# Kernel optimization log

Hardware: AMD Instinct MI355X
Metric: run time of the kernel (lower is better)

The kernel has to match this reference:

```python
import jax, jax.numpy as jnp
import numpy as np

B, N, D, H, K = 8, 128, 256, 128, 8

def setup_inputs() -> dict:
    key = jax.random.key(0)
    ks = jax.random.split(key, 6)
    E = jax.random.normal(ks[0], (B, N, D), dtype=jnp.float32)
    # kaiming_uniform-like init for linear weights
    lim1 = np.sqrt(6.0 / (2 * D))
    W1 = jax.random.uniform(ks[1], (H, 2 * D), minval=-lim1, maxval=lim1, dtype=jnp.float32)
    b1 = jnp.zeros((H,), dtype=jnp.float32)
    lim2 = np.sqrt(6.0 / H)
    W2 = jax.random.uniform(ks[2], (D, H), minval=-lim2, maxval=lim2, dtype=jnp.float32)
    b2 = jnp.zeros((D,), dtype=jnp.float32)
    q = jax.random.normal(ks[3], (K, D), dtype=jnp.float32) * (1.0 / D ** 0.5)
    return {"E": E, "W1": W1, "b1": b1, "W2": W2, "b2": b2, "q": q}

def reference(E, W1, b1, W2, b2, q):
    # phi(cat(Ei,Ej)) == relu(E_i @ W1a^T + E_j @ W1b^T + b1) @ W2^T + b2
    # Split first linear's weight to avoid materializing the [B,N,N,2D] concat.
    W1a, W1b = W1[:, :D], W1[:, D:]          # each [H, D]
    Ai = jnp.einsum('bnd,hd->bnh', E, W1a)   # [B,N,H] (row half)
    Aj = jnp.einsum('bnd,hd->bnh', E, W1b)   # [B,N,H] (col half)
    hidden = jax.nn.relu(Ai[:, :, None, :] + Aj[:, None, :, :] + b1)  # [B,N,N,H]
    # dropout is identity at inference
    # Fuse second linear with query dot: (hidden @ W2^T + b2) . q_h
    #   = hidden @ (W2^T q_h) + b2.q_h
    Wq = jnp.einsum('dh,kd->hk', W2, q)      # [H, K]
    bq = jnp.einsum('d,kd->k', b2, q)        # [K]
    logits = jnp.einsum('bijh,hk->bijh'[:0] or 'bijh,hk->bijk', hidden, Wq) + bq  # [B,N,N,K]
    M = jax.nn.sigmoid(logits).transpose(0, 3, 1, 2)  # [B,K,N,N]
    eye = jnp.eye(N, dtype=M.dtype)[None, None]
    return M * (1.0 - eye)
```

## Files before the change

kernel.cpp:

```cpp
#include <hip/hip_runtime.h>

#define PB 8
#define PN 128
#define PD 256
#define PH 128
#define PK 8
#define D2 (2*PD)

__global__ __launch_bounds__(256) void k0_prep(
        const float* __restrict__ W1, const float* __restrict__ W2,
        const float* __restrict__ b2, const float* __restrict__ q,
        float4* __restrict__ W1t4, float* __restrict__ Wq, float* __restrict__ bq)
{
    const int blk = blockIdx.x, t = threadIdx.x;
    if (blk < 64) {
        __shared__ float sm[32][33];
        const int h0 = (blk >> 4) * 32;
        const int d0 = (blk & 15) * 32;
        const int tx = t & 31, ty = t >> 5;
        #pragma unroll
        for (int r = 0; r < 4; ++r)
            sm[ty + 8 * r][tx] = W1[(h0 + ty + 8 * r) * D2 + d0 + tx];
        __syncthreads();
        const int hl = t & 31, dql = t >> 5;
        float4 w = make_float4(sm[hl][dql * 4 + 0], sm[hl][dql * 4 + 1],
                               sm[hl][dql * 4 + 2], sm[hl][dql * 4 + 3]);
        W1t4[((d0 >> 2) + dql) * PH + h0 + hl] = w;
    } else {
        __shared__ float qs[PD];
        __shared__ float red[256];
        const int k = blk - 64;
        qs[t] = q[k * PD + t];
        __syncthreads();
        if (t < PH) {
            float acc = 0.f;
            #pragma unroll 4
            for (int d = 0; d < PD; ++d)
                acc = fmaf(W2[d * PH + t], qs[d], acc);
            Wq[t * PK + k] = acc;
        }
        red[t] = b2[t] * qs[t];
        __syncthreads();
        for (int st = 128; st > 0; st >>= 1) {
            if (t < st) red[t] += red[t + st];
            __syncthreads();
        }
        if (t == 0) bq[k] = red[0];
    }
}

__global__ __launch_bounds__(256) void k1_proj(
        const float* __restrict__ E, const float* __restrict__ b1,
        const float4* __restrict__ W1t4,
        float* __restrict__ Ai, float* __restrict__ Ajt)
{
    __shared__ float es[8 * PD];
    const int blk = blockIdx.x, t = threadIdx.x;
    const int b    = blk >> 5;
    const int part = (blk >> 4) & 1;
    const int ng   = blk & 15;
    const int h    = t & (PH - 1);
    const int s    = t >> 7;

    const float* eb = E + (b * PN + ng * 8) * PD;
    #pragma unroll
    for (int r = 0; r < 8; ++r) es[r * PD + t] = eb[r * PD + t];
    __syncthreads();

    const float4* wp = W1t4 + (part * 64) * PH + h;
    const float* e0 = es + (s * 4 + 0) * PD;
    const float* e1 = e0 + PD;
    const float* e2 = e1 + PD;
    const float* e3 = e2 + PD;

    float a0 = 0.f, a1 = 0.f, a2 = 0.f, a3 = 0.f;
    #pragma unroll 4
    for (int dq = 0; dq < 64; ++dq) {
        const float4 w  = wp[dq * PH];
        const float4 p0 = *reinterpret_cast<const float4*>(e0 + dq * 4);
        const float4 p1 = *reinterpret_cast<const float4*>(e1 + dq * 4);
        const float4 p2 = *reinterpret_cast<const float4*>(e2 + dq * 4);
        const float4 p3 = *reinterpret_cast<const float4*>(e3 + dq * 4);
        a0 = fmaf(w.x, p0.x, a0); a0 = fmaf(w.y, p0.y, a0);
        a0 = fmaf(w.z, p0.z, a0); a0 = fmaf(w.w, p0.w, a0);
        a1 = fmaf(w.x, p1.x, a1); a1 = fmaf(w.y, p1.y, a1);
        a1 = fmaf(w.z, p1.z, a1); a1 = fmaf(w.w, p1.w, a1);
        a2 = fmaf(w.x, p2.x, a2); a2 = fmaf(w.y, p2.y, a2);
        a2 = fmaf(w.z, p2.z, a2); a2 = fmaf(w.w, p2.w, a2);
        a3 = fmaf(w.x, p3.x, a3); a3 = fmaf(w.y, p3.y, a3);
        a3 = fmaf(w.z, p3.z, a3); a3 = fmaf(w.w, p3.w, a3);
    }

    const int n0 = ng * 8 + s * 4;
    if (part == 0) {
        const float bb = b1[h];
        Ai[(b * PN + n0 + 0) * PH + h] = a0 + bb;
        Ai[(b * PN + n0 + 1) * PH + h] = a1 + bb;
        Ai[(b * PN + n0 + 2) * PH + h] = a2 + bb;
        Ai[(b * PN + n0 + 3) * PH + h] = a3 + bb;
    } else {
        *reinterpret_cast<float4*>(&Ajt[(b * PH + h) * PN + n0]) =
            make_float4(a0, a1, a2, a3);
    }
}

__global__ __launch_bounds__(256) void k2_score(
        const float* __restrict__ Ai, const float* __restrict__ Ajt,
        const float* __restrict__ Wq, const float* __restrict__ bq,
        float* __restrict__ out)
{
    __shared__ float  ais[4 * PH];
    __shared__ float4 wqs[2 * PH];
    __shared__ float  bqs[PK];

    const int blk = blockIdx.x, t = threadIdx.x;
    const int b  = blk >> 5;
    const int ig = blk & 31;
    const int i0 = ig * 4;
    const int il = t >> 6;
    const int jb = t & 63;

    ais[t]       = Ai[(b * PN + i0) * PH + t];
    ais[256 + t] = Ai[(b * PN + i0) * PH + 256 + t];
    wqs[t] = reinterpret_cast<const float4*>(Wq)[t];
    if (t < PK) bqs[t] = bq[t];
    __syncthreads();

    const float* ail = ais + il * PH;
    const float* ajr = Ajt + b * PH * PN + jb;

    float acc0[PK], acc1[PK];
    #pragma unroll
    for (int k = 0; k < PK; ++k) { acc0[k] = bqs[k]; acc1[k] = bqs[k]; }

    #pragma unroll 4
    for (int hh = 0; hh < PH; ++hh) {
        const float a  = ail[hh];
        const float g0 = ajr[hh * PN];
        const float g1 = ajr[hh * PN + 64];
        const float v0 = fmaxf(a + g0, 0.f);
        const float v1 = fmaxf(a + g1, 0.f);
        const float4 wA = wqs[hh * 2];
        const float4 wB = wqs[hh * 2 + 1];
        acc0[0] = fmaf(v0, wA.x, acc0[0]); acc0[1] = fmaf(v0, wA.y, acc0[1]);
        acc0[2] = fmaf(v0, wA.z, acc0[2]); acc0[3] = fmaf(v0, wA.w, acc0[3]);
        acc0[4] = fmaf(v0, wB.x, acc0[4]); acc0[5] = fmaf(v0, wB.y, acc0[5]);
        acc0[6] = fmaf(v0, wB.z, acc0[6]); acc0[7] = fmaf(v0, wB.w, acc0[7]);
        acc1[0] = fmaf(v1, wA.x, acc1[0]); acc1[1] = fmaf(v1, wA.y, acc1[1]);
        acc1[2] = fmaf(v1, wA.z, acc1[2]); acc1[3] = fmaf(v1, wA.w, acc1[3]);
        acc1[4] = fmaf(v1, wB.x, acc1[4]); acc1[5] = fmaf(v1, wB.y, acc1[5]);
        acc1[6] = fmaf(v1, wB.z, acc1[6]); acc1[7] = fmaf(v1, wB.w, acc1[7]);
    }

    const int i = i0 + il;
    #pragma unroll
    for (int k = 0; k < PK; ++k) {
        float s0 = 1.f / (1.f + __expf(-acc0[k]));
        float s1 = 1.f / (1.f + __expf(-acc1[k]));
        if (jb == i)      s0 = 0.f;
        if (jb + 64 == i) s1 = 0.f;
        float* orow = out + ((b * PK + k) * PN + i) * PN;
        orow[jb]      = s0;
        orow[jb + 64] = s1;
    }
}

extern "C" void kernel_launch(void* const* d_in, const int* in_sizes, int n_in,
                              void* d_out, int out_size, void* d_ws, size_t ws_size,
                              hipStream_t stream) {
    const float* E  = (const float*)d_in[0];
    const float* W1 = (const float*)d_in[1];
    const float* b1 = (const float*)d_in[2];
    const float* W2 = (const float*)d_in[3];
    const float* b2 = (const float*)d_in[4];
    const float* q  = (const float*)d_in[5];

    float*  Ai   = (float*)d_ws;
    float*  Ajt  = Ai + PB * PN * PH;
    float4* W1t4 = (float4*)(Ajt + PB * PH * PN);
    float*  Wq   = (float*)(W1t4 + 128 * PH);
    float*  bq   = Wq + PH * PK;

    k0_prep<<<72,  256, 0, stream>>>(W1, W2, b2, q, W1t4, Wq, bq);
    k1_proj<<<256, 256, 0, stream>>>(E, b1, W1t4, Ai, Ajt);
    k2_score<<<256, 256, 0, stream>>>(Ai, Ajt, Wq, bq, (float*)d_out);
}
```

Before: 103.8 us.

## Drop LDS staging in projection and score kernels, use wave-uniform global loads

The projection kernel no longer stages E rows in shared memory. Each thread now computes two rows instead of four, and the grid doubles to 512 blocks. The row base is made wave-uniform with readfirstlane so E can be fetched through scalar or broadcast loads. The score kernel also drops its shared staging of Ai, Wq and bq and the barrier, reading them directly from global memory with uniform addresses, and the unroll factor is raised to 8. This removes the LDS copies and syncs and adds parallelism, at the cost of more global or scalar-cache traffic and less reuse of W1 per thread.

Result: no change. 101.9 us (-1.8%).

```diff
diff --git a/kernel.cpp b/kernel.cpp
--- a/kernel.cpp
+++ b/kernel.cpp
@@ -54,94 +54,74 @@
         const float4* __restrict__ W1t4,
         float* __restrict__ Ai, float* __restrict__ Ajt)
 {
-    __shared__ float es[8 * PD];
     const int blk = blockIdx.x, t = threadIdx.x;
-    const int b    = blk >> 5;
-    const int part = (blk >> 4) & 1;
-    const int ng   = blk & 15;
+    const int b    = blk >> 6;
+    const int part = (blk >> 5) & 1;
+    const int rg   = blk & 31;
     const int h    = t & (PH - 1);
     const int s    = t >> 7;
+    const int n    = rg * 4 + 2 * s;
 
-    const float* eb = E + (b * PN + ng * 8) * PD;
-    #pragma unroll
-    for (int r = 0; r < 8; ++r) es[r * PD + t] = eb[r * PD + t];
-    __syncthreads();
+    const int ebase = __builtin_amdgcn_readfirstlane((b * PN + n) * PD);
+    const float* e0 = E + ebase;
+    const float* e1 = e0 + PD;
+    const float4* wp = W1t4 + (part * 64) * PH + h;
 
-    const float4* wp = W1t4 + (part * 64) * PH + h;
-    const float* e0 = es + (s * 4 + 0) * PD;
-    const float* e1 = e0 + PD;
-    const float* e2 = e1 + PD;
-    const float* e3 = e2 + PD;
-
-    float a0 = 0.f, a1 = 0.f, a2 = 0.f, a3 = 0.f;
-    #pragma unroll 4
+    float a0 = 0.f, a1 = 0.f;
+    #pragma unroll 8
     for (int dq = 0; dq < 64; ++dq) {
         const float4 w  = wp[dq * PH];
         const float4 p0 = *reinterpret_cast<const float4*>(e0 + dq * 4);
         const float4 p1 = *reinterpret_cast<const float4*>(e1 + dq * 4);
-        const float4 p2 = *reinterpret_cast<const float4*>(e2 + dq * 4);
-        const float4 p3 = *reinterpret_cast<const float4*>(e3 + dq * 4);
         a0 = fmaf(w.x, p0.x, a0); a0 = fmaf(w.y, p0.y, a0);
         a0 = fmaf(w.z, p0.z, a0); a0 = fmaf(w.w, p0.w, a0);
         a1 = fmaf(w.x, p1.x, a1); a1 = fmaf(w.y, p1.y, a1);
         a1 = fmaf(w.z, p1.z, a1); a1 = fmaf(w.w, p1.w, a1);
-        a2 = fmaf(w.x, p2.x, a2); a2 = fmaf(w.y, p2.y, a2);
-        a2 = fmaf(w.z, p2.z, a2); a2 = fmaf(w.w, p2.w, a2);
-        a3 = fmaf(w.x, p3.x, a3); a3 = fmaf(w.y, p3.y, a3);
-        a3 = fmaf(w.z, p3.z, a3); a3 = fmaf(w.w, p3.w, a3);
     }
 
-    const int n0 = ng * 8 + s * 4;
     if (part == 0) {
         const float bb = b1[h];
-        Ai[(b * PN + n0 + 0) * PH + h] = a0 + bb;
-        Ai[(b * PN + n0 + 1) * PH + h] = a1 + bb;
-        Ai[(b * PN + n0 + 2) * PH + h] = a2 + bb;
-        Ai[(b * PN + n0 + 3) * PH + h] = a3 + bb;
+        Ai[(b * PN + n + 0) * PH + h] = a0 + bb;
+        Ai[(b * PN + n + 1) * PH + h] = a1 + bb;
     } else {
-        *reinterpret_cast<float4*>(&Ajt[(b * PH + h) * PN + n0]) =
-            make_float4(a0, a1, a2, a3);
+        *reinterpret_cast<float2*>(&Ajt[(b * PH + h) * PN + n]) =
+            make_float2(a0, a1);
     }
 }
 
 __global__ __launch_bounds__(256) void k2_score(
         const float* __restrict__ Ai, const float* __restrict__ Ajt,
-        const float* __restrict__ Wq, const float* __restrict__ bq,
+        const float4* __restrict__ Wq4, const float* __restrict__ bq,
         float* __restrict__ out)
 {
-    __shared__ float  ais[4 * PH];
-    __shared__ float4 wqs[2 * PH];
-    __shared__ float  bqs[PK];
-
     const int blk = blockIdx.x, t = threadIdx.x;
     const int b  = blk >> 5;
-    const int ig = blk & 31;
-    const int i0 = ig * 4;
+    const int i0 = (blk & 31) * 4;
     const int il = t >> 6;
     const int jb = t & 63;
+    const int i  = i0 + il;
 
-    ais[t]       = Ai[(b * PN + i0) * PH + t];
-    ais[256 + t] = Ai[(b * PN + i0) * PH + 256 + t];
-    wqs[t] = reinterpret_cast<const float4*>(Wq)[t];
-    if (t < PK) bqs[t] = bq[t];
-    __syncthreads();
-
-    const float* ail = ais + il * PH;
-    const float* ajr = Ajt + b * PH * PN + jb;
+    const int aib = __builtin_amdgcn_readfirstlane((b * PN + i) * PH);
+    const float* ai = Ai + aib;
+    const float* aj = Ajt + b * PH * PN + jb;
 
     float acc0[PK], acc1[PK];
-    #pragma unroll
-    for (int k = 0; k < PK; ++k) { acc0[k] = bqs[k]; acc1[k] = bqs[k]; }
+    const float q0 = bq[0], q1 = bq[1], q2 = bq[2], q3 = bq[3];
+    const float q4 = bq[4], q5 = bq[5], q6 = bq[6], q7 = bq[7];
+    acc0[0]=q0; acc0[1]=q1; acc0[2]=q2; acc0[3]=q3;
+    acc0[4]=q4; acc0[5]=q5; acc0[6]=q6; acc0[7]=q7;
+    acc1[0]=q0; acc1[1]=q1; acc1[2]=q2; acc1[3]=q3;
+    acc1[4]=q4; acc1[5]=q5; acc1[6]=q6; acc1[7]=q7;
 
-    #pragma unroll 4
+    #pragma unroll 8
     for (int hh = 0; hh < PH; ++hh) {
-        const float a  = ail[hh];
-        const float g0 = ajr[hh * PN];
-        const float g1 = ajr[hh * PN + 64];
+        const float a  = ai[hh];
+        const float g0 = aj[hh * PN];
+        const float g1 = aj[hh * PN + 64];
         const float v0 = fmaxf(a + g0, 0.f);
         const float v1 = fmaxf(a + g1, 0.f);
-        const float4 wA = wqs[hh * 2];
-        const float4 wB = wqs[hh * 2 + 1];
+        const float4 wA = Wq4[hh * 2];
+        const float4 wB = Wq4[hh * 2 + 1];
         acc0[0] = fmaf(v0, wA.x, acc0[0]); acc0[1] = fmaf(v0, wA.y, acc0[1]);
         acc0[2] = fmaf(v0, wA.z, acc0[2]); acc0[3] = fmaf(v0, wA.w, acc0[3]);
         acc0[4] = fmaf(v0, wB.x, acc0[4]); acc0[5] = fmaf(v0, wB.y, acc0[5]);
@@ -152,7 +132,6 @@
         acc1[6] = fmaf(v1, wB.z, acc1[6]); acc1[7] = fmaf(v1, wB.w, acc1[7]);
     }
 
-    const int i = i0 + il;
     #pragma unroll
     for (int k = 0; k < PK; ++k) {
         float s0 = 1.f / (1.f + __expf(-acc0[k]));
@@ -182,6 +161,6 @@
     float*  bq   = Wq + PH * PK;
 
     k0_prep<<<72,  256, 0, stream>>>(W1, W2, b2, q, W1t4, Wq, bq);
-    k1_proj<<<256, 256, 0, stream>>>(E, b1, W1t4, Ai, Ajt);
-    k2_score<<<256, 256, 0, stream>>>(Ai, Ajt, Wq, bq, (float*)d_out);
+    k1_proj<<<512, 256, 0, stream>>>(E, b1, W1t4, Ai, Ajt);
+    k2_score<<<256, 256, 0, stream>>>(Ai, Ajt, (const float4*)Wq, bq, (float*)d_out);
 }
```
